# Performance work log

Measured on AMD Instinct MI355X. Metric: run time of the kernel, lower is better.

Reference implementation:

```python
import jax, jax.numpy as jnp
import numpy as np
from jax.scipy.ndimage import map_coordinates

B, G, C, H, W = 8, 16, 1, 384, 384
K = 3                    # rectangular (box) kernel size
KV = float(K * K)        # kernel volume (sum of ones kernel)
LBD = 1.0
SMOOTH_DR = 1e-5         # monai LNCC default smooth_dr (smooth_nr = 0)


def setup_inputs() -> dict:
    key = jax.random.key(0)
    k1, k2 = jax.random.split(key)
    images = jax.random.normal(k1, (B, G, C, H, W), dtype=jnp.float32)
    warps = jax.random.normal(k2, (B, G, 2, H, W), dtype=jnp.float32)
    return {"images": images, "warps": warps}


def _warp2d(images, flow):
    """Bilinear warp. images [N,C,H,W], flow [N,2,H,W] (pixel displacements,
    channel 0 = x/width, channel 1 = y/height). Border-clamped sampling."""
    gy, gx = jnp.meshgrid(jnp.arange(H, dtype=images.dtype),
                          jnp.arange(W, dtype=images.dtype), indexing="ij")
    cy = gy[None] + flow[:, 1]   # [N,H,W]
    cx = gx[None] + flow[:, 0]   # [N,H,W]

    def samp(img2d, cy_, cx_):
        return map_coordinates(img2d, [cy_, cx_], order=1, mode="nearest")

    # vmap over channels, then over batch
    per_img = jax.vmap(samp, in_axes=(0, None, None))        # over C
    return jax.vmap(per_img, in_axes=(0, 0, 0))(images, cy, cx)  # over N


def _box_sum(x):
    """3x3 box-filter sum with zero padding (SAME). x: [N,C,H,W]."""
    k = jnp.ones((1, 1, K, K), x.dtype)
    return jax.lax.conv_general_dilated(
        x, k, window_strides=(1, 1), padding="SAME",
        dimension_numbers=("NCHW", "OIHW", "NCHW"))


def _lncc_loss(pred, target):
    """monai LocalNormalizedCrossCorrelationLoss (rectangular kernel)."""
    t_sum = _box_sum(target)
    p_sum = _box_sum(pred)
    t2_sum = _box_sum(target * target)
    p2_sum = _box_sum(pred * pred)
    tp_sum = _box_sum(target * pred)
    t_avg = t_sum / KV
    p_avg = p_sum / KV
    cross = tp_sum - p_avg * t_sum
    t_var = jnp.maximum(t2_sum - t_avg * t_sum, 0.0)
    p_var = jnp.maximum(p2_sum - p_avg * p_sum, 0.0)
    ncc = (cross * cross) / (t_var * p_var + SMOOTH_DR)
    return -jnp.mean(ncc)


def reference(images, warps):
    imgs = images.reshape(B * G, C, H, W)
    flow = warps.reshape(B * G, 2, H, W)
    warped = _warp2d(imgs, flow)                       # [B*G,C,H,W]
    template = jnp.mean(warped, axis=0, keepdims=True)  # [1,C,H,W]
    lncc = _lncc_loss(jnp.broadcast_to(template, warped.shape), warped)
    # Grad2d('l2') on warps [B,G,2,H,W]
    dy = warps[:, :, :, 1:, :] - warps[:, :, :, :-1, :]
    dx = warps[:, :, :, :, 1:] - warps[:, :, :, :, :-1]
    g2 = (jnp.mean(dx * dx) + jnp.mean(dy * dy)) / 2.0
    return lncc + LBD * g2
```

## Files before the change

### kernel.cpp

```cpp
#include <hip/hip_runtime.h>
#include <hip/hip_fp16.h>

#define HH 384
#define WW 384
#define HW (HH * WW)
#define NIMG 128
#define NPIX (NIMG * HW)
#define GRAD_CNT 37650432.0

#define K1_TH 16
#define K1_M  4
#define K1_NT (HH / K1_TH)
#define K1_SROWS (K1_TH + 2 * K1_M)
#define K1_LSH 432
#define NP_G (K1_NT * NIMG)

#define K2_SPLIT 8

#define K3_T 32
#define K3_NX (WW / K3_T)
#define K3_TILES (K3_NX * (HH / K3_T))
#define NP_N (K3_TILES * NIMG)

__device__ inline int pad_off(int x) { return x + 4 * (x >> 5); }

__device__ inline void block_reduce_store_256(float v, float* dst) {
    #pragma unroll
    for (int o = 32; o > 0; o >>= 1) v += __shfl_down(v, o);
    __shared__ float s[4];
    int wave = threadIdx.x >> 6, lane = threadIdx.x & 63;
    if (lane == 0) s[wave] = v;
    __syncthreads();
    if (threadIdx.x == 0) *dst = s[0] + s[1] + s[2] + s[3];
}

__device__ inline void block_reduce_store2_256(float v0, float v1,
                                               float* d0, float* d1) {
    #pragma unroll
    for (int o = 32; o > 0; o >>= 1) {
        v0 += __shfl_down(v0, o);
        v1 += __shfl_down(v1, o);
    }
    __shared__ float s0[4], s1[4];
    int wave = threadIdx.x >> 6, lane = threadIdx.x & 63;
    if (lane == 0) { s0[wave] = v0; s1[wave] = v1; }
    __syncthreads();
    if (threadIdx.x == 0) {
        *d0 = s0[0] + s0[1] + s0[2] + s0[3];
        *d1 = s1[0] + s1[1] + s1[2] + s1[3];
    }
}

__global__ __launch_bounds__(256, 7) void warp_grad_kernel(
        const float* __restrict__ images, const float* __restrict__ warps,
        __half* __restrict__ warped, float* __restrict__ partialsG) {
    __shared__ __half simg[K1_SROWS * K1_LSH];
    int n = blockIdx.y;
    int yt = blockIdx.x;
    int y0 = yt * K1_TH;
    int ys0 = max(0, y0 - K1_M);
    int ys1 = min(HH - 1, y0 + K1_TH - 1 + K1_M);
    int cnt = ys1 - ys0 + 1;
    const float* img = images + (size_t)n * HW;
    int tid = threadIdx.x;

    for (int i = tid; i < cnt * 96; i += 256) {
        int r = i / 96, gg = i - r * 96;
        int x0 = gg * 4;
        float4 v = *(const float4*)(img + (ys0 + r) * WW + x0);
        union { __half2 h2[2]; uint2 u; } pk;
        pk.h2[0] = __floats2half2_rn(v.x, v.y);
        pk.h2[1] = __floats2half2_rn(v.z, v.w);
        *(uint2*)(simg + r * K1_LSH + pad_off(x0)) = pk.u;
    }
    __syncthreads();

    const float* flow0 = warps + (size_t)n * 2 * HW;
    const float* flow1 = flow0 + HW;
    float g = 0.f;

    #pragma unroll 2
    for (int gi = 0; gi < 6; ++gi) {
        int p4 = gi * 256 + tid;
        int r = p4 / 96;
        int c4 = p4 - r * 96;
        int x0 = c4 * 4;
        int y = y0 + r;
        int base = y * WW + x0;

        float4 f0 = *(const float4*)(flow0 + base);
        float4 f1 = *(const float4*)(flow1 + base);

        float a0 = __shfl_down(f0.x, 1);
        float a1 = __shfl_down(f1.x, 1);
        if (c4 == 95) {
            a0 = f0.w; a1 = f1.w;
        } else if ((tid & 63) == 63) {
            a0 = flow0[base + 4]; a1 = flow1[base + 4];
        }

        float d;
        d = f0.y - f0.x; g += d * d;  d = f1.y - f1.x; g += d * d;
        d = f0.z - f0.y; g += d * d;  d = f1.z - f1.y; g += d * d;
        d = f0.w - f0.z; g += d * d;  d = f1.w - f1.z; g += d * d;
        d = a0 - f0.w;   g += d * d;  d = a1 - f1.w;   g += d * d;
        if (y + 1 < HH) {
            float4 b0 = *(const float4*)(flow0 + base + WW);
            float4 b1 = *(const float4*)(flow1 + base + WW);
            d = b0.x - f0.x; g += d * d;  d = b1.x - f1.x; g += d * d;
            d = b0.y - f0.y; g += d * d;  d = b1.y - f1.y; g += d * d;
            d = b0.z - f0.z; g += d * d;  d = b1.z - f1.z; g += d * d;
            d = b0.w - f0.w; g += d * d;  d = b1.w - f1.w; g += d * d;
        }

        float fxa[4] = {f0.x, f0.y, f0.z, f0.w};
        float fya[4] = {f1.x, f1.y, f1.z, f1.w};
        float o[4];
        #pragma unroll
        for (int j = 0; j < 4; ++j) {
            float cx = (float)(x0 + j) + fxa[j];
            float cy = (float)y + fya[j];
            float flx = floorf(cx), fly = floorf(cy);
            float wx = cx - flx, wy = cy - fly;
            int xi = (int)flx, yi = (int)fly;
            int x0c = min(max(xi, 0), WW - 1), x1c = min(max(xi + 1, 0), WW - 1);
            int y0c = min(max(yi, 0), HH - 1), y1c = min(max(yi + 1, 0), HH - 1);
            float v00, v01, v10, v11;
            if (y0c >= ys0 && y1c <= ys1) {
                const __half* r0 = simg + (y0c - ys0) * K1_LSH;
                const __half* r1 = simg + (y1c - ys0) * K1_LSH;
                int oa = pad_off(x0c), ob = pad_off(x1c);
                v00 = __half2float(r0[oa]); v01 = __half2float(r0[ob]);
                v10 = __half2float(r1[oa]); v11 = __half2float(r1[ob]);
            } else {
                v00 = img[y0c * WW + x0c]; v01 = img[y0c * WW + x1c];
                v10 = img[y1c * WW + x0c]; v11 = img[y1c * WW + x1c];
            }
            float top = v00 + wx * (v01 - v00);
            float bot = v10 + wx * (v11 - v10);
            o[j] = top + wy * (bot - top);
        }
        union { __half2 h2[2]; uint2 u; } cv;
        cv.h2[0] = __floats2half2_rn(o[0], o[1]);
        cv.h2[1] = __floats2half2_rn(o[2], o[3]);
        *(uint2*)(warped + (size_t)n * HW + base) = cv.u;
    }
    block_reduce_store_256(g, &partialsG[(size_t)n * K1_NT + yt]);
}

__global__ __launch_bounds__(256) void template_part_kernel(
        const __half* __restrict__ warped, float* __restrict__ tpart) {
    int p8 = blockIdx.x * 256 + threadIdx.x;
    int q = blockIdx.y;
    const __half* p = warped + (size_t)q * (NIMG / K2_SPLIT) * HW + p8 * 8;
    float s[8] = {0, 0, 0, 0, 0, 0, 0, 0};
    #pragma unroll 4
    for (int nn = 0; nn < NIMG / K2_SPLIT; ++nn) {
        union { uint4 u; __half2 h2[4]; } cv;
        cv.u = *(const uint4*)(p + (size_t)nn * HW);
        #pragma unroll
        for (int k = 0; k < 4; ++k) {
            float2 f = __half22float2(cv.h2[k]);
            s[2 * k] += f.x; s[2 * k + 1] += f.y;
        }
    }
    float* dst = tpart + (size_t)q * HW + p8 * 8;
    *(float4*)dst       = make_float4(s[0], s[1], s[2], s[3]);
    *(float4*)(dst + 4) = make_float4(s[4], s[5], s[6], s[7]);
}

__global__ __launch_bounds__(256) void template_combine_kernel(
        const float* __restrict__ tpart, float* __restrict__ templ) {
    int p4 = blockIdx.x * 256 + threadIdx.x;
    float sx = 0, sy = 0, sz = 0, sw = 0;
    #pragma unroll
    for (int pl = 0; pl < K2_SPLIT; ++pl) {
        float4 a = *(const float4*)(tpart + (size_t)pl * HW + p4 * 4);
        sx += a.x; sy += a.y; sz += a.z; sw += a.w;
    }
    const float sc = 1.f / (float)NIMG;
    *(float4*)(templ + p4 * 4) = make_float4(sx * sc, sy * sc, sz * sc, sw * sc);
}

__global__ __launch_bounds__(256) void lncc_kernel(
        const __half* __restrict__ warped, const float* __restrict__ templ,
        float* __restrict__ partialsN) {
    __shared__ float st0[34][40];
    __shared__ float st1[34][40];
    __shared__ float sp[34][40];
    int n0 = blockIdx.y;
    int n1 = n0 + 64;
    int tile = blockIdx.x;
    int tyt = tile / K3_NX, txt = tile - tyt * K3_NX;
    int oy0 = tyt * K3_T, ox0 = txt * K3_T;
    const __half* t0 = warped + (size_t)n0 * HW;
    const __half* t1 = warped + (size_t)n1 * HW;
    int tid = threadIdx.x;

    for (int i = tid; i < 34 * 10; i += 256) {
        int ly = i / 10, c = i - (i / 10) * 10;
        int gy = oy0 + ly - 1;
        int gx = ox0 - 4 + c * 4;
        float4 tv0 = {0, 0, 0, 0}, tv1 = {0, 0, 0, 0}, pv = {0, 0, 0, 0};
        if (gy >= 0 && gy < HH && gx >= 0 && gx + 3 < WW) {
            union { uint2 u; __half2 h2[2]; } cv;
            cv.u = *(const uint2*)(t0 + gy * WW + gx);
            float2 lo = __half22float2(cv.h2[0]);
            float2 hi = __half22float2(cv.h2[1]);
            tv0 = make_float4(lo.x, lo.y, hi.x, hi.y);
            cv.u = *(const uint2*)(t1 + gy * WW + gx);
            lo = __half22float2(cv.h2[0]);
            hi = __half22float2(cv.h2[1]);
            tv1 = make_float4(lo.x, lo.y, hi.x, hi.y);
            pv = *(const float4*)(templ + gy * WW + gx);
        }
        *(float4*)&st0[ly][c * 4] = tv0;
        *(float4*)&st1[ly][c * 4] = tv1;
        *(float4*)&sp[ly][c * 4] = pv;
    }
    __syncthreads();

    int tx = tid & 7, ty = tid >> 3;
    int xb = tx * 4;
    float cA[6] = {0,0,0,0,0,0}, cA2[6] = {0,0,0,0,0,0}, cAP[6] = {0,0,0,0,0,0};
    float cB[6] = {0,0,0,0,0,0}, cB2[6] = {0,0,0,0,0,0}, cBP[6] = {0,0,0,0,0,0};
    float cP[6] = {0,0,0,0,0,0}, cP2[6] = {0,0,0,0,0,0};
    #pragma unroll
    for (int r = 0; r < 3; ++r) {
        float ta0 = st0[ty + r][xb + 3];
        float4 ta4 = *(const float4*)&st0[ty + r][xb + 4];
        float ta5 = st0[ty + r][xb + 8];
        float tb0 = st1[ty + r][xb + 3];
        float4 tb4 = *(const float4*)&st1[ty + r][xb + 4];
        float tb5 = st1[ty + r][xb + 8];
        float p0 = sp[ty + r][xb + 3];
        float4 p4 = *(const float4*)&sp[ty + r][xb + 4];
        float p5 = sp[ty + r][xb + 8];
        float av[6] = {ta0, ta4.x, ta4.y, ta4.z, ta4.w, ta5};
        float bv[6] = {tb0, tb4.x, tb4.y, tb4.z, tb4.w, tb5};
        float pv[6] = {p0, p4.x, p4.y, p4.z, p4.w, p5};
        #pragma unroll
        for (int c = 0; c < 6; ++c) {
            cA[c] += av[c]; cB[c] += bv[c]; cP[c] += pv[c];
            cA2[c] = fmaf(av[c], av[c], cA2[c]);
            cB2[c] = fmaf(bv[c], bv[c], cB2[c]);
            cP2[c] = fmaf(pv[c], pv[c], cP2[c]);
            cAP[c] = fmaf(av[c], pv[c], cAP[c]);
            cBP[c] = fmaf(bv[c], pv[c], cBP[c]);
        }
    }
    const float inv9 = 1.f / 9.f;
    float ncc0 = 0.f, ncc1 = 0.f;
    #pragma unroll
    for (int j = 0; j < 4; ++j) {
        float ps = cP[j] + cP[j + 1] + cP[j + 2];
        float p2s = cP2[j] + cP2[j + 1] + cP2[j + 2];
        float pvar = fmaxf(p2s - (ps * inv9) * ps, 0.f);
        {
            float ts = cA[j] + cA[j + 1] + cA[j + 2];
            float t2s = cA2[j] + cA2[j + 1] + cA2[j + 2];
            float tps = cAP[j] + cAP[j + 1] + cAP[j + 2];
            float cross = tps - (ps * inv9) * ts;
            float tvar = fmaxf(t2s - (ts * inv9) * ts, 0.f);
            ncc0 += (cross * cross) / (tvar * pvar + 1e-5f);
        }
        {
            float ts = cB[j] + cB[j + 1] + cB[j + 2];
            float t2s = cB2[j] + cB2[j + 1] + cB2[j + 2];
            float tps = cBP[j] + cBP[j + 1] + cBP[j + 2];
            float cross = tps - (ps * inv9) * ts;
            float tvar = fmaxf(t2s - (ts * inv9) * ts, 0.f);
            ncc1 += (cross * cross) / (tvar * pvar + 1e-5f);
        }
    }
    block_reduce_store2_256(ncc0, ncc1,
                            &partialsN[(size_t)n0 * K3_TILES + tile],
                            &partialsN[(size_t)n1 * K3_TILES + tile]);
}

__global__ __launch_bounds__(1024) void finalize_kernel(
        const float* __restrict__ pN, const float* __restrict__ pG,
        float* __restrict__ out) {
    double accN = 0.0, accG = 0.0;
    for (int i = threadIdx.x; i < NP_N; i += 1024) accN += (double)pN[i];
    for (int i = threadIdx.x; i < NP_G; i += 1024) accG += (double)pG[i];
    #pragma unroll
    for (int o = 32; o > 0; o >>= 1) {
        accN += __shfl_down(accN, o);
        accG += __shfl_down(accG, o);
    }
    __shared__ double sN[16], sG[16];
    int wave = threadIdx.x >> 6, lane = threadIdx.x & 63;
    if (lane == 0) { sN[wave] = accN; sG[wave] = accG; }
    __syncthreads();
    if (threadIdx.x == 0) {
        double tN = 0.0, tG = 0.0;
        #pragma unroll
        for (int w = 0; w < 16; ++w) { tN += sN[w]; tG += sG[w]; }
        double lncc = -(tN / (double)NPIX);
        double g2 = tG / (2.0 * GRAD_CNT);
        out[0] = (float)(lncc + g2);
    }
}

extern "C" void kernel_launch(void* const* d_in, const int* in_sizes, int n_in,
                              void* d_out, int out_size, void* d_ws, size_t ws_size,
                              hipStream_t stream) {
    const float* images = (const float*)d_in[0];
    const float* warps  = (const float*)d_in[1];
    float* out = (float*)d_out;

    __half* warped  = (__half*)d_ws;
    float* fbase    = (float*)((char*)d_ws + (size_t)NPIX * 2);
    float* partialsN = fbase;
    float* partialsG = partialsN + NP_N;
    float* tpart     = partialsG + NP_G;
    float* templ     = tpart + (size_t)K2_SPLIT * HW;

    warp_grad_kernel<<<dim3(K1_NT, NIMG), dim3(256), 0, stream>>>(
        images, warps, warped, partialsG);
    template_part_kernel<<<dim3(HW / 8 / 256, K2_SPLIT), dim3(256), 0, stream>>>(
        warped, tpart);
    template_combine_kernel<<<dim3(HW / 4 / 256), dim3(256), 0, stream>>>(
        tpart, templ);
    lncc_kernel<<<dim3(K3_TILES, 64), dim3(256), 0, stream>>>(
        warped, templ, partialsN);
    finalize_kernel<<<dim3(1), dim3(1024), 0, stream>>>(
        partialsN, partialsG, out);
}
```

Before: 115.2 us.

## Store neighbor-paired half2 image rows in LDS and clamp coordinates before sampling

The warp kernel now stages each image row in shared memory as half2 pairs (pixel, right neighbor), so one bilinear tap row is a single 32-bit LDS load instead of two padded half loads. Coordinates are clamped to the image in float first, which folds the border handling into one path, and a per-thread check sends all four samples to either the LDS path or the global fallback. The row tile shrinks from 16 to 8 rows with a 3-row margin, so each block loops 3 times instead of 6. Trade-offs: LDS per row doubles and halo rows take up a larger share of each tile; the smaller margin and whole-thread fallback may send more samples to global memory; clamping before the floor also changes the interpolation weights at the borders.

```diff
diff --git a/kernel.cpp b/kernel.cpp
--- a/kernel.cpp
+++ b/kernel.cpp
@@ -8,11 +8,10 @@
 #define NPIX (NIMG * HW)
 #define GRAD_CNT 37650432.0
 
-#define K1_TH 16
-#define K1_M  4
+#define K1_TH 8
+#define K1_M  3
 #define K1_NT (HH / K1_TH)
 #define K1_SROWS (K1_TH + 2 * K1_M)
-#define K1_LSH 432
 #define NP_G (K1_NT * NIMG)
 
 #define K2_SPLIT 8
@@ -22,8 +21,6 @@
 #define K3_TILES (K3_NX * (HH / K3_T))
 #define NP_N (K3_TILES * NIMG)
 
-__device__ inline int pad_off(int x) { return x + 4 * (x >> 5); }
-
 __device__ inline void block_reduce_store_256(float v, float* dst) {
     #pragma unroll
     for (int o = 32; o > 0; o >>= 1) v += __shfl_down(v, o);
@@ -54,7 +51,7 @@
 __global__ __launch_bounds__(256, 7) void warp_grad_kernel(
         const float* __restrict__ images, const float* __restrict__ warps,
         __half* __restrict__ warped, float* __restrict__ partialsG) {
-    __shared__ __half simg[K1_SROWS * K1_LSH];
+    __shared__ __half2 simg[K1_SROWS * WW];
     int n = blockIdx.y;
     int yt = blockIdx.x;
     int y0 = yt * K1_TH;
@@ -67,11 +64,17 @@
     for (int i = tid; i < cnt * 96; i += 256) {
         int r = i / 96, gg = i - r * 96;
         int x0 = gg * 4;
-        float4 v = *(const float4*)(img + (ys0 + r) * WW + x0);
-        union { __half2 h2[2]; uint2 u; } pk;
-        pk.h2[0] = __floats2half2_rn(v.x, v.y);
-        pk.h2[1] = __floats2half2_rn(v.z, v.w);
-        *(uint2*)(simg + r * K1_LSH + pad_off(x0)) = pk.u;
+        const float* rowp = img + (ys0 + r) * WW + x0;
+        float4 v = *(const float4*)rowp;
+        float nb = __shfl_down(v.x, 1);
+        if (gg == 95) nb = v.w;
+        else if ((tid & 63) == 63) nb = rowp[4];
+        union { __half2 h[4]; uint4 u; } pk;
+        pk.h[0] = __floats2half2_rn(v.x, v.y);
+        pk.h[1] = __floats2half2_rn(v.y, v.z);
+        pk.h[2] = __floats2half2_rn(v.z, v.w);
+        pk.h[3] = __floats2half2_rn(v.w, nb);
+        *(uint4*)(simg + r * WW + x0) = pk.u;
     }
     __syncthreads();
 
@@ -79,8 +82,8 @@
     const float* flow1 = flow0 + HW;
     float g = 0.f;
 
-    #pragma unroll 2
-    for (int gi = 0; gi < 6; ++gi) {
+    #pragma unroll
+    for (int gi = 0; gi < 3; ++gi) {
         int p4 = gi * 256 + tid;
         int r = p4 / 96;
         int c4 = p4 - r * 96;
@@ -115,30 +118,45 @@
 
         float fxa[4] = {f0.x, f0.y, f0.z, f0.w};
         float fya[4] = {f1.x, f1.y, f1.z, f1.w};
+
+        float cxc[4], cyc[4];
+        #pragma unroll
+        for (int j = 0; j < 4; ++j) {
+            cxc[j] = fminf(fmaxf((float)(x0 + j) + fxa[j], 0.f), 383.f);
+            cyc[j] = fminf(fmaxf((float)y + fya[j], 0.f), 383.f);
+        }
+        bool ok = true;
+        #pragma unroll
+        for (int j = 0; j < 4; ++j) {
+            int yi = (int)cyc[j];
+            ok = ok && (yi >= ys0) && (yi < ys1);
+        }
+
         float o[4];
-        #pragma unroll
-        for (int j = 0; j < 4; ++j) {
-            float cx = (float)(x0 + j) + fxa[j];
-            float cy = (float)y + fya[j];
-            float flx = floorf(cx), fly = floorf(cy);
-            float wx = cx - flx, wy = cy - fly;
-            int xi = (int)flx, yi = (int)fly;
-            int x0c = min(max(xi, 0), WW - 1), x1c = min(max(xi + 1, 0), WW - 1);
-            int y0c = min(max(yi, 0), HH - 1), y1c = min(max(yi + 1, 0), HH - 1);
-            float v00, v01, v10, v11;
-            if (y0c >= ys0 && y1c <= ys1) {
-                const __half* r0 = simg + (y0c - ys0) * K1_LSH;
-                const __half* r1 = simg + (y1c - ys0) * K1_LSH;
-                int oa = pad_off(x0c), ob = pad_off(x1c);
-                v00 = __half2float(r0[oa]); v01 = __half2float(r0[ob]);
-                v10 = __half2float(r1[oa]); v11 = __half2float(r1[ob]);
-            } else {
-                v00 = img[y0c * WW + x0c]; v01 = img[y0c * WW + x1c];
-                v10 = img[y1c * WW + x0c]; v11 = img[y1c * WW + x1c];
+        if (ok) {
+            #pragma unroll
+            for (int j = 0; j < 4; ++j) {
+                int xi = (int)cxc[j], yi = (int)cyc[j];
+                float wx = cxc[j] - (float)xi, wy = cyc[j] - (float)yi;
+                const __half2* rp = simg + (yi - ys0) * WW + xi;
+                float2 tp = __half22float2(rp[0]);
+                float2 bt = __half22float2(rp[WW]);
+                float top = fmaf(wx, tp.y - tp.x, tp.x);
+                float bot = fmaf(wx, bt.y - bt.x, bt.x);
+                o[j] = fmaf(wy, bot - top, top);
             }
-            float top = v00 + wx * (v01 - v00);
-            float bot = v10 + wx * (v11 - v10);
-            o[j] = top + wy * (bot - top);
+        } else {
+            #pragma unroll
+            for (int j = 0; j < 4; ++j) {
+                int xi = (int)cxc[j], yi = (int)cyc[j];
+                float wx = cxc[j] - (float)xi, wy = cyc[j] - (float)yi;
+                int x1 = min(xi + 1, WW - 1), y1 = min(yi + 1, HH - 1);
+                float v00 = img[yi * WW + xi], v01 = img[yi * WW + x1];
+                float v10 = img[y1 * WW + xi], v11 = img[y1 * WW + x1];
+                float top = fmaf(wx, v01 - v00, v00);
+                float bot = fmaf(wx, v11 - v10, v10);
+                o[j] = fmaf(wy, bot - top, top);
+            }
         }
         union { __half2 h2[2]; uint2 u; } cv;
         cv.h2[0] = __floats2half2_rn(o[0], o[1]);
```

New measurement: 116.1 us. Within noise of the previous version (+0.9%).
